# Performance work log

Hardware: AMD Instinct MI355X
Metric: run time of the kernel (lower is better)

## Reference

```python
import jax, jax.numpy as jnp
from jax import lax
import numpy as np

STRIDE = 2
EXT_PAD = (2, 2)  # computed in __init__: (total_pad - inter_pad)//2 split symmetrically


def setup_inputs() -> dict:
    key = jax.random.key(0)
    k1, k2, k3 = jax.random.split(key, 3)
    x = jax.random.normal(k1, (32, 256, 32, 32), dtype=jnp.float32)
    # Conv kernel in OIHW layout: [out_chs, in_chs, kh, kw]
    W = jax.random.normal(k2, (128, 256, 4, 4), dtype=jnp.float32) * 0.05
    b = jax.random.normal(k3, (128,), dtype=jnp.float32) * 0.01
    return {"x": x, "W": W, "b": b}


def reference(x, W, b):
    # _Interpad: insert (stride-1) zeros between every pair of adjacent spatial
    # elements (not after the last one): new_size = (size-1)*stride + 1.
    B, C, H, Wd = x.shape
    s = STRIDE
    stuffed = jnp.zeros((B, C, (H - 1) * s + 1, (Wd - 1) * s + 1), dtype=x.dtype)
    stuffed = stuffed.at[:, :, ::s, ::s].set(x)
    # external zero padding
    p = EXT_PAD
    padded = jnp.pad(stuffed, ((0, 0), (0, 0), p, p))
    # standard (cross-correlation) conv, stride 1, dilation 1, valid padding
    y = lax.conv_general_dilated(
        padded, W,
        window_strides=(1, 1),
        padding='VALID',
        rhs_dilation=(1, 1),
        dimension_numbers=('NCHW', 'OIHW', 'NCHW'),
    )
    return y + b[None, :, None, None]
```

## Files before the change

### kernel.cpp

```cpp
#include <hip/hip_runtime.h>


typedef float  f32x4  __attribute__((ext_vector_type(4)));
typedef short  short8 __attribute__((ext_vector_type(8)));
typedef unsigned short ushort4v __attribute__((ext_vector_type(4)));
typedef unsigned short ushort8v __attribute__((ext_vector_type(8)));

__device__ __forceinline__ unsigned short f2bf(float f) {
    unsigned u = __builtin_bit_cast(unsigned, f);
    u += 0x7fffu + ((u >> 16) & 1u);
    return (unsigned short)(u >> 16);
}

__device__ __forceinline__ void ld_lds16(const unsigned short* g, unsigned short* l) {
    __builtin_amdgcn_global_load_lds(
        (const __attribute__((address_space(1))) unsigned int*)g,
        (__attribute__((address_space(3))) unsigned int*)l,
        16, 0, 0);
}

#define XP_U 288
#define XP_G 9792
#define XP_N 313344
#define WP_G 8192
#define WP_PI 262144
#define WROW 1040
#define WBUFS 8320

__global__ __launch_bounds__(256) void prepack_w2(const float* __restrict__ W,
                                                  unsigned short* __restrict__ wp) {
    int t = blockIdx.x * 256 + threadIdx.x;
    int o = t >> 8, c = t & 255;
    int g = c >> 3, c8 = c & 7;
    const float4* src = (const float4*)(W + (size_t)(o * 256 + c) * 16);
    float4 q0 = src[0], q1 = src[1], q2 = src[2], q3 = src[3];
    float rows[4][4] = {{q0.x,q0.y,q0.z,q0.w},{q1.x,q1.y,q1.z,q1.w},
                        {q2.x,q2.y,q2.z,q2.w},{q3.x,q3.y,q3.z,q3.w}};
    #pragma unroll
    for (int pi = 0; pi < 2; ++pi)
    #pragma unroll
    for (int pj = 0; pj < 2; ++pj)
    #pragma unroll
    for (int du = 0; du < 2; ++du)
    #pragma unroll
    for (int dv = 0; dv < 2; ++dv)
        wp[pi*WP_PI + g*WP_G + pj*4096 + (du*2+dv)*1024 + o*8 + c8] =
            f2bf(rows[pi+2*du][pj+2*dv]);
}

__global__ __launch_bounds__(256) void prepack_x(const float* __restrict__ x,
                                                 unsigned short* __restrict__ xp) {
    __shared__ unsigned short xt[256 * 32];
    const int tid = threadIdx.x;
    const int up  = blockIdx.x;
    const int n   = blockIdx.y;
    const bool interior = (up >= 1 && up <= 32);

    if (interior) {
        const int u = up - 1;
        #pragma unroll
        for (int k = 0; k < 8; ++k) {
            int idx4 = tid + k * 256;
            int c = idx4 >> 3, v4 = idx4 & 7;
            float4 val = *(const float4*)(x + ((size_t)(n*256 + c)*32 + u)*32 + v4*4);
            ushort4v s = { f2bf(val.x), f2bf(val.y), f2bf(val.z), f2bf(val.w) };
            *(ushort4v*)&xt[c*32 + v4*4] = s;
        }
        __syncthreads();
    }

    #pragma unroll
    for (int s = 0; s < 5; ++s) {
        int id = tid + s * 256;
        if (id < 1152) {
            int g = id / 36, vp = id % 36;
            ushort8v o8 = {0,0,0,0,0,0,0,0};
            if (interior && vp >= 1 && vp <= 32) {
                #pragma unroll
                for (int e = 0; e < 8; ++e)
                    o8[e] = xt[(g*8 + e)*32 + (vp - 1)];
            }
            *(ushort8v*)&xp[(size_t)n*XP_N + g*XP_G + up*XP_U + vp*8] = o8;
        }
    }
}

__global__ __launch_bounds__(256, 2) void tconv_main(
    const unsigned short* __restrict__ xp,
    const unsigned short* __restrict__ wp,
    const float* __restrict__ bias,
    float* __restrict__ out)
{
    __shared__ __align__(16) unsigned short lds[33280];
    unsigned short* wsh0 = lds;

    const int tid  = threadIdx.x;
    const int lane = tid & 63;
    const int w    = tid >> 6;
    const int pjw  = w >> 1;
    const int half = w & 1;
    const int lg   = lane >> 4;
    const int ln   = lane & 15;
    const int du   = lg >> 1, dv = lg & 1;

    const int bid = blockIdx.x;
    const int wg  = (bid & 7) * 64 + (bid >> 3);
    const int n   = wg >> 4;
    const int aq  = (wg >> 1) & 7;
    const int pi  = wg & 1;
    const int a0  = aq * 4;

    const unsigned short* xpb = xp + (size_t)n * XP_N + (a0 + pi) * XP_U;
    const unsigned short* wpb = wp + pi * WP_PI;

    int xoff[4];
    #pragma unroll
    for (int jj = 0; jj < 4; ++jj) {
        int rr = half * 2 + (jj >> 1) + du;
        int vv = (jj & 1) * 16 + ln + pjw + dv;
        xoff[jj] = rr * XP_U + vv * 8;
    }
    const int wfoff = (pjw * 4 + lg) * WROW + ln * 8;

    f32x4 acc[8][4];
    #pragma unroll
    for (int i = 0; i < 8; ++i)
        #pragma unroll
        for (int jj = 0; jj < 4; ++jj)
            acc[i][jj] = (f32x4){0.f, 0.f, 0.f, 0.f};

    short8 xA[4], xB[4];

#define STAGE_W(CH, WBUF)                                                    \
    { const unsigned short* ws_ = wpb + (size_t)(CH) * WP_G;                 \
      unsigned short* wd_ = wsh0 + (WBUF) * WBUFS;                           \
      _Pragma("unroll")                                                      \
      for (int s_ = 0; s_ < 4; ++s_) {                                       \
          int r_ = w * 2 + (s_ >> 1), h_ = s_ & 1;                           \
          ld_lds16(ws_ + r_ * 1024 + h_ * 512 + lane * 8,                    \
                   wd_ + r_ * WROW + h_ * 512); } }

#define LOAD_X(CH, XS)                                                      \
    { const unsigned short* xs_ = xpb + (size_t)(CH) * XP_G;                 \
      _Pragma("unroll")                                                      \
      for (int jj_ = 0; jj_ < 4; ++jj_)                                      \
          XS[jj_] = *(const short8*)(xs_ + xoff[jj_]); }

#define CHUNK(BUF, XS, CH, VMN, DO_W, DO_X)                                  \
    {                                                                        \
        __builtin_amdgcn_sched_barrier(0);                                   \
        asm volatile("s_waitcnt vmcnt(" #VMN ")" ::: "memory");              \
        __builtin_amdgcn_s_barrier();                                        \
        __builtin_amdgcn_sched_barrier(0);                                   \
        if (DO_W) STAGE_W((CH) + 3, ((BUF) + 3) & 3);                        \
        const unsigned short* wb_ = wsh0 + (BUF) * WBUFS + wfoff;            \
        _Pragma("unroll")                                                    \
        for (int i_ = 0; i_ < 8; ++i_) {                                     \
            short8 av_ = *(const short8*)&wb_[i_ * 128];                     \
            _Pragma("unroll")                                                \
            for (int jj_ = 0; jj_ < 4; ++jj_)                                \
                acc[i_][jj_] = __builtin_amdgcn_mfma_f32_16x16x32_bf16(      \
                    av_, XS[jj_], acc[i_][jj_], 0, 0, 0);                    \
        }                                                                    \
        if (DO_X) LOAD_X((CH) + 2, XS);                                      \
    }

    STAGE_W(0, 0);
    STAGE_W(1, 1);
    __builtin_amdgcn_sched_barrier(0);
    LOAD_X(0, xA);
    __builtin_amdgcn_sched_barrier(0);
    STAGE_W(2, 2);
    __builtin_amdgcn_sched_barrier(0);
    LOAD_X(1, xB);
    __builtin_amdgcn_sched_barrier(0);

    for (int ch4 = 0; ch4 < 28; ch4 += 4) {
        CHUNK(0, xA, ch4 + 0, 8, 1, 1);
        CHUNK(1, xB, ch4 + 1, 8, 1, 1);
        CHUNK(2, xA, ch4 + 2, 8, 1, 1);
        CHUNK(3, xB, ch4 + 3, 8, 1, 1);
    }
    CHUNK(0, xA, 28, 8, 1, 1);
    CHUNK(1, xB, 29, 8, 0, 1);
    CHUNK(2, xA, 30, 4, 0, 0);
    CHUNK(3, xB, 31, 0, 0, 0);

#undef CHUNK
#undef LOAD_X
#undef STAGE_W

    float* epi = (float*)lds;
    #pragma unroll
    for (int i = 0; i < 8; ++i) {
        __syncthreads();
        f32x4 bv = *(const f32x4*)&bias[i * 16 + lg * 4];
        #pragma unroll
        for (int jj = 0; jj < 4; ++jj) {
            int ar = half * 2 + (jj >> 1);
            int b  = (jj & 1) * 16 + ln;
            #pragma unroll
            for (int r = 0; r < 4; ++r)
                epi[((lg * 4 + r) * 8 + ar * 2 + pjw) * 33 + b] = acc[i][jj][r] + bv[r];
        }
        __syncthreads();
        #pragma unroll
        for (int k = 0; k < 4; ++k) {
            int f   = tid + k * 256;
            int row = f >> 4;
            int q   = f & 15;
            float4 v;
            v.x = epi[(row * 2 + 0) * 33 + q * 2 + 0];
            v.y = epi[(row * 2 + 1) * 33 + q * 2 + 0];
            v.z = epi[(row * 2 + 0) * 33 + q * 2 + 1];
            v.w = epi[(row * 2 + 1) * 33 + q * 2 + 1];
            int o     = i * 16 + (row >> 2);
            int i_out = 2 * (a0 + (row & 3)) + pi;
            *(float4*)&out[(((size_t)n * 128 + o) * 64 + i_out) * 64 + q * 4] = v;
        }
    }
}

__global__ __launch_bounds__(256) void prepack_w(const float* __restrict__ W,
                                                 unsigned short* __restrict__ Wp) {
    int t = blockIdx.x * 256 + threadIdx.x;
    int o = t >> 8, c = t & 255;
    const float4* src = (const float4*)(W + (size_t)(o * 256 + c) * 16);
    float4 q0 = src[0], q1 = src[1], q2 = src[2], q3 = src[3];
    float rows[4][4] = {{q0.x,q0.y,q0.z,q0.w},{q1.x,q1.y,q1.z,q1.w},
                        {q2.x,q2.y,q2.z,q2.w},{q3.x,q3.y,q3.z,q3.w}};
    #pragma unroll
    for (int pi = 0; pi < 2; ++pi)
    #pragma unroll
    for (int pj = 0; pj < 2; ++pj)
    #pragma unroll
    for (int du = 0; du < 2; ++du)
    #pragma unroll
    for (int dv = 0; dv < 2; ++dv)
        Wp[((((pi*2+pj)*4 + du*2+dv)*128 + o)*256) + c] = f2bf(rows[pi+2*du][pj+2*dv]);
}

template<bool PRE>
__global__ __launch_bounds__(512, 2) void tconv_mfma(
    const float* __restrict__ x, const float* __restrict__ W,
    const unsigned short* __restrict__ Wp, const float* __restrict__ bias,
    float* __restrict__ out)
{
    __shared__ __align__(16) unsigned short xsh[2][9 * 34 * 8];
    __shared__ __align__(16) unsigned short wsh[2][2 * 4 * 128 * 8];

    const int tid = threadIdx.x;
    const int bid = blockIdx.x;
    const int pi  = bid & 1;
    const int aq  = (bid >> 1) & 3;
    const int n   = bid >> 3;
    const int a0  = aq * 8;
    const int u0  = a0 + pi - 1;

    const int l   = tid & 63;
    const int w   = tid >> 6;
    const int pjw = w >> 2;
    const int q   = w & 3;
    const int lg  = l >> 4;
    const int ln  = l & 15;

    const int sv = tid & 31;
    const int sg = tid >> 5;

    f32x4 acc[8][4];
    #pragma unroll
    for (int i = 0; i < 8; ++i)
        #pragma unroll
        for (int jj = 0; jj < 4; ++jj)
            acc[i][jj] = (f32x4){0.f, 0.f, 0.f, 0.f};

    float    xv[5];
    ushort4v wv[4];
    float4   wa[2], wb[2];

    auto stage_load = [&](int ch) {
        const int c0 = ch * 8;
        #pragma unroll
        for (int s = 0; s < 5; ++s) {
            int p = sg * 5 + s;
            if (p < 72) {
                int c = p & 7, rr = p >> 3;
                int u = u0 + rr;
                xv[s] = ((unsigned)u < 32u)
                      ? x[((n*256 + c0 + c)*32 + u)*32 + sv] : 0.f;
            }
        }
        if (PRE) {
            #pragma unroll
            for (int k = 0; k < 4; ++k) {
                int uu = tid + k * 512;
                int chalf = uu & 1, o = (uu >> 1) & 127;
                int sub = (uu >> 8) & 3, pjq = (uu >> 10) & 1;
                wv[k] = *(const ushort4v*)&Wp[(((pi*2 + pjq)*4 + sub)*128 + o)*256
                                              + c0 + chalf*4];
            }
        } else {
            #pragma unroll
            for (int k = 0; k < 2; ++k) {
                int pr = tid + k * 512;
                int o = pr >> 3, c = pr & 7;
                const float* base = W + ((o*256 + c0 + c) << 4) + pi*4;
                wa[k] = *(const float4*)base;
                wb[k] = *(const float4*)(base + 8);
            }
        }
    };

    auto stage_write = [&](int buf) {
        #pragma unroll
        for (int s = 0; s < 5; ++s) {
            int p = sg * 5 + s;
            if (p < 72) {
                int c = p & 7, rr = p >> 3;
                xsh[buf][(rr*34 + sv + 1)*8 + c] = f2bf(xv[s]);
            }
        }
        if (tid < 144) {
            int pr = tid >> 1;
            int rr = pr >> 3, c = pr & 7;
            int cw = (tid & 1) * 33;
            xsh[buf][(rr*34 + cw)*8 + c] = 0;
        }
        if (PRE) {
            #pragma unroll
            for (int k = 0; k < 4; ++k) {
                int uu = tid + k * 512;
                int chalf = uu & 1, o = (uu >> 1) & 127;
                int sub = (uu >> 8) & 3, pjq = (uu >> 10) & 1;
                *(ushort4v*)&wsh[buf][(((pjq*4 + sub)*128 + o)*8) + chalf*4] = wv[k];
            }
        } else {
            #pragma unroll
            for (int k = 0; k < 2; ++k) {
                int pr = tid + k * 512;
                int o = pr >> 3, c = pr & 7;
                float ra[4] = {wa[k].x, wa[k].y, wa[k].z, wa[k].w};
                float rb[4] = {wb[k].x, wb[k].y, wb[k].z, wb[k].w};
                #pragma unroll
                for (int pj2 = 0; pj2 < 2; ++pj2)
                #pragma unroll
                for (int duu = 0; duu < 2; ++duu)
                #pragma unroll
                for (int dvv = 0; dvv < 2; ++dvv) {
                    float val = duu ? rb[pj2 + 2*dvv] : ra[pj2 + 2*dvv];
                    wsh[buf][(((pj2*4 + duu*2 + dvv)*128 + o)*8) + c] = f2bf(val);
                }
            }
        }
    };

    stage_load(0);
    stage_write(0);
    __syncthreads();

    for (int ch = 0; ch < 32; ++ch) {
        const int cur = ch & 1;
        if (ch + 1 < 32) stage_load(ch + 1);

        short8 bfr[4];
        #pragma unroll
        for (int jj = 0; jj < 4; ++jj) {
            int arow = q*2 + (jj >> 1);
            int b    = (jj & 1)*16 + ln;
            int rr   = arow + (lg >> 1);
            int cw   = b + pjw + (lg & 1);
            bfr[jj]  = *(const short8*)&xsh[cur][(rr*34 + cw)*8];
        }
        #pragma unroll
        for (int i = 0; i < 8; ++i) {
            short8 av = *(const short8*)&wsh[cur][((pjw*4 + lg)*128 + i*16 + ln)*8];
            #pragma unroll
            for (int jj = 0; jj < 4; ++jj)
                acc[i][jj] = __builtin_amdgcn_mfma_f32_16x16x32_bf16(
                                 av, bfr[jj], acc[i][jj], 0, 0, 0);
        }

        if (ch + 1 < 32) stage_write(cur ^ 1);
        __syncthreads();
    }

    #pragma unroll
    for (int i = 0; i < 8; ++i) {
        const f32x4 bv = *(const f32x4*)&bias[i*16 + lg*4];
        #pragma unroll
        for (int jj = 0; jj < 4; ++jj) {
            int arow  = q*2 + (jj >> 1);
            int b     = (jj & 1)*16 + ln;
            int i_out = 2*(a0 + arow) + pi;
            int j_out = 2*b + pjw;
            int o0    = i*16 + lg*4;
            int base  = ((n*128 + o0)*64 + i_out)*64 + j_out;
            #pragma unroll
            for (int r = 0; r < 4; ++r)
                out[base + r*4096] = acc[i][jj][r] + bv[r];
        }
    }
}

extern "C" void kernel_launch(void* const* d_in, const int* in_sizes, int n_in,
                              void* d_out, int out_size, void* d_ws, size_t ws_size,
                              hipStream_t stream) {
    const float* x    = (const float*)d_in[0];
    const float* W    = (const float*)d_in[1];
    const float* bias = (const float*)d_in[2];
    float* out        = (float*)d_out;

    const size_t wp2_bytes = (size_t)2 * WP_PI * 2;
    const size_t xp_bytes  = (size_t)32 * XP_N * 2;
    if (ws_size >= wp2_bytes + xp_bytes) {
        unsigned short* wp2 = (unsigned short*)d_ws;
        unsigned short* xpp = (unsigned short*)((char*)d_ws + wp2_bytes);
        prepack_w2<<<128, 256, 0, stream>>>(W, wp2);
        prepack_x<<<dim3(34, 32), 256, 0, stream>>>(x, xpp);
        tconv_main<<<512, 256, 0, stream>>>(xpp, wp2, bias, out);
    } else if (ws_size >= (size_t)4*4*128*256*2) {
        unsigned short* Wp = (unsigned short*)d_ws;
        prepack_w<<<128, 256, 0, stream>>>(W, Wp);
        tconv_mfma<true><<<256, 512, 0, stream>>>(x, W, Wp, bias, out);
    } else {
        tconv_mfma<false><<<256, 512, 0, stream>>>(x, W, nullptr, bias, out);
    }
}
```

Measured before the change: 55.32 us.

## Shrink weight ring to three LDS buffers for three blocks per CU

Cuts the weight staging ring in LDS from four buffers to three and shortens the prefetch distance by one chunk, so the kernel can declare three resident blocks per CU instead of two. The MFMA loop is wrapped in s_setprio to favour issuing math while other waves load. The epilogue LDS layout is permuted so readback uses paired float2 loads. The tighter register budget may cause spills, the shorter prefetch may expose load latency, and some float2 reads land on odd-word addresses.

```diff
diff --git a/kernel.cpp b/kernel.cpp
--- a/kernel.cpp
+++ b/kernel.cpp
@@ -85,13 +85,13 @@
     }
 }
 
-__global__ __launch_bounds__(256, 2) void tconv_main(
+__global__ __launch_bounds__(256, 3) void tconv_main(
     const unsigned short* __restrict__ xp,
     const unsigned short* __restrict__ wp,
     const float* __restrict__ bias,
     float* __restrict__ out)
 {
-    __shared__ __align__(16) unsigned short lds[33280];
+    __shared__ __align__(16) unsigned short lds[24960];
     unsigned short* wsh0 = lds;
 
     const int tid  = threadIdx.x;
@@ -146,14 +146,15 @@
       for (int jj_ = 0; jj_ < 4; ++jj_)                                      \
           XS[jj_] = *(const short8*)(xs_ + xoff[jj_]); }
 
-#define CHUNK(BUF, XS, CH, VMN, DO_W, DO_X)                                  \
+#define CHUNK(BUF, SBUF, XS, CH, VMN, DO_W, DO_X)                            \
     {                                                                        \
         __builtin_amdgcn_sched_barrier(0);                                   \
         asm volatile("s_waitcnt vmcnt(" #VMN ")" ::: "memory");              \
         __builtin_amdgcn_s_barrier();                                        \
         __builtin_amdgcn_sched_barrier(0);                                   \
-        if (DO_W) STAGE_W((CH) + 3, ((BUF) + 3) & 3);                        \
+        if (DO_W) STAGE_W((CH) + 2, SBUF);                                   \
         const unsigned short* wb_ = wsh0 + (BUF) * WBUFS + wfoff;            \
+        __builtin_amdgcn_s_setprio(1);                                       \
         _Pragma("unroll")                                                    \
         for (int i_ = 0; i_ < 8; ++i_) {                                     \
             short8 av_ = *(const short8*)&wb_[i_ * 128];                     \
@@ -162,29 +163,29 @@
                 acc[i_][jj_] = __builtin_amdgcn_mfma_f32_16x16x32_bf16(      \
                     av_, XS[jj_], acc[i_][jj_], 0, 0, 0);                    \
         }                                                                    \
+        __builtin_amdgcn_s_setprio(0);                                       \
         if (DO_X) LOAD_X((CH) + 2, XS);                                      \
     }
 
     STAGE_W(0, 0);
-    STAGE_W(1, 1);
     __builtin_amdgcn_sched_barrier(0);
     LOAD_X(0, xA);
     __builtin_amdgcn_sched_barrier(0);
-    STAGE_W(2, 2);
+    STAGE_W(1, 1);
     __builtin_amdgcn_sched_barrier(0);
     LOAD_X(1, xB);
     __builtin_amdgcn_sched_barrier(0);
 
-    for (int ch4 = 0; ch4 < 28; ch4 += 4) {
-        CHUNK(0, xA, ch4 + 0, 8, 1, 1);
-        CHUNK(1, xB, ch4 + 1, 8, 1, 1);
-        CHUNK(2, xA, ch4 + 2, 8, 1, 1);
-        CHUNK(3, xB, ch4 + 3, 8, 1, 1);
-    }
-    CHUNK(0, xA, 28, 8, 1, 1);
-    CHUNK(1, xB, 29, 8, 0, 1);
-    CHUNK(2, xA, 30, 4, 0, 0);
-    CHUNK(3, xB, 31, 0, 0, 0);
+    for (int c6 = 0; c6 < 30; c6 += 6) {
+        CHUNK(0, 2, xA, c6 + 0, 8, 1, 1);
+        CHUNK(1, 0, xB, c6 + 1, 8, 1, 1);
+        CHUNK(2, 1, xA, c6 + 2, 8, 1, 1);
+        CHUNK(0, 2, xB, c6 + 3, 8, 1, 1);
+        CHUNK(1, 0, xA, c6 + 4, 8, 1, 1);
+        CHUNK(2, 1, xB, c6 + 5, 8, 1, 1);
+    }
+    CHUNK(0, 2, xA, 30, 8, 0, 0);
+    CHUNK(1, 0, xB, 31, 4, 0, 0);
 
 #undef CHUNK
 #undef LOAD_X
@@ -201,20 +202,19 @@
             int b  = (jj & 1) * 16 + ln;
             #pragma unroll
             for (int r = 0; r < 4; ++r)
-                epi[((lg * 4 + r) * 8 + ar * 2 + pjw) * 33 + b] = acc[i][jj][r] + bv[r];
+                epi[((r * 4 + lg) * 8 + ar * 2 + pjw) * 33 + b] = acc[i][jj][r] + bv[r];
         }
         __syncthreads();
         #pragma unroll
         for (int k = 0; k < 4; ++k) {
-            int f   = tid + k * 256;
-            int row = f >> 4;
-            int q   = f & 15;
-            float4 v;
-            v.x = epi[(row * 2 + 0) * 33 + q * 2 + 0];
-            v.y = epi[(row * 2 + 1) * 33 + q * 2 + 0];
-            v.z = epi[(row * 2 + 0) * 33 + q * 2 + 1];
-            v.w = epi[(row * 2 + 1) * 33 + q * 2 + 1];
-            int o     = i * 16 + (row >> 2);
+            int f    = tid + k * 256;
+            int row  = f >> 4;
+            int q    = f & 15;
+            float2 A = *(const float2*)&epi[(row * 2 + 0) * 33 + q * 2];
+            float2 B = *(const float2*)&epi[(row * 2 + 1) * 33 + q * 2];
+            float4 v = { A.x, B.x, A.y, B.y };
+            int olp   = row >> 2;
+            int o     = i * 16 + ((olp & 3) << 2) + (olp >> 2);
             int i_out = 2 * (a0 + (row & 3)) + pi;
             *(float4*)&out[(((size_t)n * 128 + o) * 64 + i_out) * 64 + q * 4] = v;
         }
```

After: 187.0 us (median of 3 runs). 238% more time.
